# Kernel optimization log

Measured on AMD Instinct MI355X. Metric: run time of the kernel, lower is better.

## Reference

```python
import jax, jax.numpy as jnp
import numpy as np

E = 128   # embed_dim
H = 8     # num_heads
N, T, LQ, LK = 32, 50, 64, 64


def setup_inputs() -> dict:
    rng = jax.random.key(0)
    ks = jax.random.split(rng, 9)
    xav = np.sqrt(2.0 / (E + E)).astype(np.float32)  # xavier_normal for square E x E
    return {
        "query": jax.random.normal(ks[0], (N, T, LQ, E), jnp.float32),
        "key": jax.random.normal(ks[1], (N, T, LK, E), jnp.float32),
        "value": jax.random.normal(ks[2], (N, T, LK, E), jnp.float32),
        "key_padding_mask": jax.random.bernoulli(ks[3], 0.1, (N, T, LK)),
        "Wq": jax.random.normal(ks[4], (E, E), jnp.float32) * xav,
        "bq": jnp.zeros((E,), jnp.float32),
        "Wk": jax.random.normal(ks[5], (E, E), jnp.float32) * xav,
        "bk": jnp.zeros((E,), jnp.float32),
        "Wv": jax.random.normal(ks[6], (E, E), jnp.float32) * xav,
        "bv": jnp.zeros((E,), jnp.float32),
        "Wo": jax.random.normal(ks[7], (E, E), jnp.float32) * xav,
        "bo": jnp.zeros((E,), jnp.float32),
    }


def reference(query, key, value, key_padding_mask, Wq, bq, Wk, bk, Wv, bv, Wo, bo):
    b, t, lq, _ = query.shape
    lk = key.shape[2]
    # linear projections (torch Linear: x @ W.T + b)
    q = (query @ Wq.T + bq).reshape(b, t, lq, H, -1)   # [b,T,Lq,h,d]
    k = (key @ Wk.T + bk).reshape(b, t, lk, H, -1)     # [b,T,Lk,h,d]
    v = (value @ Wv.T + bv).reshape(b, t, lk, H, -1)   # [b,T,Lk,h,d]
    scale = 1.0 / np.sqrt(q.shape[-1]).astype(np.float32)
    attn = jnp.einsum('bTlhd,bTthd->bThlt', q, k) * scale  # [b,T,h,Lq,Lk]
    mask = key_padding_mask[:, :, None, None, :]            # [b,T,1,1,Lk]
    attn = jnp.where(mask, -jnp.inf, attn)
    attn = jax.nn.softmax(attn, axis=-1)
    attn = jnp.nan_to_num(attn, nan=0.0)                    # fully-masked rows -> 0
    out = jnp.einsum('bThlt,bTthd->bTlhd', attn, v)
    out = out.reshape(b, t, lq, -1) @ Wo.T + bo             # [b,T,Lq,E]
    # match torch output layout for attn: [head, b, T, Lq, Lk]
    return out, jnp.transpose(attn, (2, 0, 1, 3, 4))
```

## Files before the change

kernel.cpp:

```cpp
#include <hip/hip_runtime.h>
#include <hip/hip_bf16.h>


#define NBT 1600
#define OUT0_ELEMS 13107200L

typedef __attribute__((ext_vector_type(8))) short bf16x8;
typedef __attribute__((ext_vector_type(4))) short bf16x4;
typedef __attribute__((ext_vector_type(4))) float f32x4;
typedef __attribute__((ext_vector_type(4))) unsigned short u16x4;

__device__ __forceinline__ unsigned short f2b(float f) {
  union { float f; unsigned u; } v; v.f = f;
  unsigned r = v.u + 0x7FFFu + ((v.u >> 16) & 1u);
  return (unsigned short)(r >> 16);
}
__device__ __forceinline__ float b2f(unsigned short s) {
  union { unsigned u; float f; } v; v.u = ((unsigned)s) << 16;
  return v.f;
}
__device__ __forceinline__ bf16x4 pack4(f32x4 v) {
  bf16x4 r;
  r[0] = (short)f2b(v[0]); r[1] = (short)f2b(v[1]);
  r[2] = (short)f2b(v[2]); r[3] = (short)f2b(v[3]);
  return r;
}

#if defined(__has_builtin)
#if __has_builtin(__builtin_amdgcn_mfma_f32_16x16x16bf16_1k)
#define HAVE_MFMA16_1K 1
#endif
#endif

__device__ __forceinline__ f32x4 mfma16(bf16x4 a, bf16x4 b, f32x4 c) {
#ifdef HAVE_MFMA16_1K
  return __builtin_amdgcn_mfma_f32_16x16x16bf16_1k(a, b, c, 0, 0, 0);
#else
  f32x4 d;
  asm volatile("v_mfma_f32_16x16x16_bf16 %0, %1, %2, %3\n\ts_nop 7\n\ts_nop 7"
               : "=v"(d)
               : "v"(a), "v"(b), "v"(c));
  return d;
#endif
}

__device__ __forceinline__ int xs_idx(int r, int c) {
  return r * 128 + (c ^ ((r & 7) << 3));
}
__device__ __forceinline__ int qk_idx(int l, int d) {
  return l * 16 + (d ^ ((l & 3) << 2));
}
__device__ __forceinline__ int ps_idx(int r, int c) {
  return r * 64 + (c ^ ((r & 7) << 3));
}

__global__ void prep_kernel(const float* __restrict__ Wq,
                            const float* __restrict__ Wk,
                            const float* __restrict__ Wv,
                            const float* __restrict__ Wo,
                            const unsigned char* __restrict__ maskp,
                            unsigned short* __restrict__ wall,
                            int* __restrict__ flag) {
  int b = blockIdx.x;
  int t = threadIdx.x;
  if (b < 256) {
    int idx = b * 256 + t;
    int m = idx >> 14, j = idx & 16383;
    const float* src = (m == 0) ? Wq : (m == 1) ? Wk : (m == 2) ? Wv : Wo;
    float s = (m == 0) ? 0.25f : 1.0f;
    wall[idx] = f2b(src[j] * s);
  } else {
    __shared__ int sb, sf;
    if (t == 0) { sb = 0; sf = 0; }
    __syncthreads();
    int bnz = 0, fcnt = 0;
    for (int i = t * 16; i < t * 16 + 16; ++i)
      if ((i & 3) && maskp[i]) bnz++;
    const unsigned int* w = (const unsigned int*)maskp;
    for (int i = t * 4; i < t * 4 + 4; ++i)
      if (w[i] == 0x3f800000u) fcnt++;
    if (bnz) atomicAdd(&sb, 1);
    if (fcnt) atomicAdd(&sf, 1);
    __syncthreads();
    if (t == 0) *flag = sf ? 2 : (sb ? 1 : 0);
  }
}

__global__ __launch_bounds__(512, 3) void fused_kernel(
    const float* __restrict__ q_in, const float* __restrict__ k_in,
    const float* __restrict__ v_in, const unsigned char* __restrict__ maskp,
    const int* __restrict__ modeFlag, const unsigned short* __restrict__ wall,
    const float* __restrict__ bq, const float* __restrict__ bk,
    const float* __restrict__ bv, const float* __restrict__ bo,
    float* __restrict__ out0, float* __restrict__ attn_out) {
  __shared__ __align__(16) unsigned short Xs0[64 * 128];
  __shared__ __align__(16) unsigned short Xs1[64 * 128];
  __shared__ __align__(16) unsigned short QKw[8 * 1024];
  __shared__ float maskS[64];

  const int tid = threadIdx.x;
  const int w = tid >> 6;
  const int lane = tid & 63;
  const int ln = lane & 15, g = lane >> 4;
  const long bT = blockIdx.x;

  unsigned short* Sw = QKw + w * 1024;

  if (tid < 64) {
    int mode = *modeFlag;
    long midx = bT * 64 + tid;
    bool mk;
    if (mode == 0)      mk = ((const int*)maskp)[midx] != 0;
    else if (mode == 1) mk = maskp[midx] != 0;
    else                mk = ((const float*)maskp)[midx] != 0.0f;
    maskS[tid] = mk ? -INFINITY : 0.0f;
  }

  const float* xsrc0 = q_in + bT * 8192;
  const float* xsrc1 = k_in + bT * 8192;
  const float* xsrc2 = v_in + bT * 8192;

  float4 xcur[4];
  #pragma unroll
  for (int it = 0; it < 4; ++it)
    xcur[it] = *(const float4*)(xsrc0 + it * 2048 + tid * 4);

  bf16x4 vk[4];
  bf16x4 aK[4], bQ[4];

  #pragma unroll
  for (int t3 = 0; t3 < 3; ++t3) {
    unsigned short* Xb = (t3 == 1) ? Xs1 : Xs0;
    #pragma unroll
    for (int it = 0; it < 4; ++it) {
      int flat = it * 2048 + tid * 4;
      int r = flat >> 7, c = flat & 127;
      float4 xv = xcur[it];
      u16x4 pk;
      pk[0] = f2b(xv.x); pk[1] = f2b(xv.y);
      pk[2] = f2b(xv.z); pk[3] = f2b(xv.w);
      *(u16x4*)&Xb[xs_idx(r, c)] = pk;
    }
    if (t3 < 2) {
      const float* nsrc = (t3 == 0) ? xsrc1 : xsrc2;
      #pragma unroll
      for (int it = 0; it < 4; ++it)
        xcur[it] = *(const float4*)(nsrc + it * 2048 + tid * 4);
    }
    __syncthreads();

    const unsigned short* wb = wall + t3 * 16384 + (w * 16 + ln) * 128 + 8 * g;
    const float* bias = (t3 == 0) ? bq : (t3 == 1) ? bk : bv;
    float bval = bias[w * 16 + ln] * ((t3 == 0) ? 0.25f : 1.0f);

    f32x4 acc[4] = {};
    #pragma unroll
    for (int ks = 0; ks < 4; ++ks) {
      bf16x8 bwk = *(const bf16x8*)(wb + ks * 32);
      bf16x8 a[4];
      #pragma unroll
      for (int ms = 0; ms < 4; ++ms)
        a[ms] = *(const bf16x8*)&Xb[xs_idx(ms * 16 + ln, ks * 32 + 8 * g)];
      #pragma unroll
      for (int ms = 0; ms < 4; ++ms)
        acc[ms] = __builtin_amdgcn_mfma_f32_16x16x32_bf16(a[ms], bwk,
                                                          acc[ms], 0, 0, 0);
    }

    #pragma unroll
    for (int ms = 0; ms < 4; ++ms) {
      if (t3 == 2) {
        f32x4 vb;
        #pragma unroll
        for (int r = 0; r < 4; ++r) vb[r] = acc[ms][r] + bval;
        vk[ms] = pack4(vb);
      } else {
        #pragma unroll
        for (int r = 0; r < 4; ++r) {
          int l = ms * 16 + 4 * g + r;
          Sw[qk_idx(l, ln)] = f2b(acc[ms][r] + bval);
        }
      }
    }
    if (t3 == 0) {
      #pragma unroll
      for (int i = 0; i < 4; ++i)
        bQ[i] = *(const bf16x4*)&Sw[qk_idx(i * 16 + ln, 4 * g)];
    } else if (t3 == 1) {
      #pragma unroll
      for (int i = 0; i < 4; ++i)
        aK[i] = *(const bf16x4*)&Sw[qk_idx(i * 16 + ln, 4 * g)];
    }
  }

  const long abase = ((long)w * NBT + bT) * 4096;
  #pragma unroll
  for (int lsub = 0; lsub < 4; ++lsub) {
    f32x4 s4[4];
    #pragma unroll
    for (int t = 0; t < 4; ++t) {
      f32x4 z = {};
      s4[t] = mfma16(aK[t], bQ[lsub], z);
    }
    float m = -INFINITY;
    #pragma unroll
    for (int t = 0; t < 4; ++t) {
      f32x4 mvt = *(const f32x4*)&maskS[t * 16 + 4 * g];
      #pragma unroll
      for (int r = 0; r < 4; ++r) {
        float sv = s4[t][r] + mvt[r];
        s4[t][r] = sv;
        m = fmaxf(m, sv);
      }
    }
    m = fmaxf(m, __shfl_xor(m, 16, 64));
    m = fmaxf(m, __shfl_xor(m, 32, 64));
    float sum = 0.f;
    #pragma unroll
    for (int t = 0; t < 4; ++t)
      #pragma unroll
      for (int r = 0; r < 4; ++r) {
        float p = (m == -INFINITY) ? 0.f : __expf(s4[t][r] - m);
        s4[t][r] = p;
        sum += p;
      }
    sum += __shfl_xor(sum, 16, 64);
    sum += __shfl_xor(sum, 32, 64);
    float inv = (sum > 0.f) ? 1.f / sum : 0.f;

    bf16x4 pa4[4];
    #pragma unroll
    for (int t = 0; t < 4; ++t) {
      f32x4 ps;
      #pragma unroll
      for (int r = 0; r < 4; ++r) ps[r] = s4[t][r] * inv;
      pa4[t] = pack4(ps);
    }

    #pragma unroll
    for (int t = 0; t < 4; ++t)
      *(u16x4*)&Sw[ps_idx(ln, t * 16 + 4 * g)] = *(const u16x4*)&pa4[t];
    #pragma unroll
    for (int j = 0; j < 4; ++j) {
      int row = 4 * j + g;
      u16x4 pv = *(const u16x4*)&Sw[ps_idx(row, 4 * ln)];
      f32x4 o;
      o[0] = b2f(pv[0]); o[1] = b2f(pv[1]);
      o[2] = b2f(pv[2]); o[3] = b2f(pv[3]);
      *(f32x4*)&attn_out[abase + (long)(lsub * 16 + row) * 64 + 4 * ln] = o;
    }

    f32x4 oacc = {};
    #pragma unroll
    for (int t = 0; t < 4; ++t) oacc = mfma16(pa4[t], vk[t], oacc);
    #pragma unroll
    for (int r = 0; r < 4; ++r)
      Xs1[xs_idx(lsub * 16 + 4 * g + r, w * 16 + ln)] = f2b(oacc[r]);
  }

  __syncthreads();

  {
    const unsigned short* wo = wall + 3 * 16384 + (w * 16 + ln) * 128 + 8 * g;
    float bov = bo[w * 16 + ln];

    f32x4 acc[4] = {};
    #pragma unroll
    for (int ks = 0; ks < 4; ++ks) {
      bf16x8 bwk = *(const bf16x8*)(wo + ks * 32);
      bf16x8 a[4];
      #pragma unroll
      for (int ms = 0; ms < 4; ++ms)
        a[ms] = *(const bf16x8*)&Xs1[xs_idx(ms * 16 + ln, ks * 32 + 8 * g)];
      #pragma unroll
      for (int ms = 0; ms < 4; ++ms)
        acc[ms] = __builtin_amdgcn_mfma_f32_16x16x32_bf16(a[ms], bwk,
                                                          acc[ms], 0, 0, 0);
    }
    #pragma unroll
    for (int ms = 0; ms < 4; ++ms)
      #pragma unroll
      for (int r = 0; r < 4; ++r)
        out0[(bT * 64 + ms * 16 + 4 * g + r) * 128 + w * 16 + ln] =
            acc[ms][r] + bov;
  }
}

extern "C" void kernel_launch(void* const* d_in, const int* in_sizes, int n_in,
                              void* d_out, int out_size, void* d_ws,
                              size_t ws_size, hipStream_t stream) {
  (void)in_sizes; (void)n_in; (void)out_size; (void)ws_size;
  const float* query = (const float*)d_in[0];
  const float* key   = (const float*)d_in[1];
  const float* value = (const float*)d_in[2];
  const unsigned char* mask = (const unsigned char*)d_in[3];
  const float* Wq = (const float*)d_in[4];
  const float* bq = (const float*)d_in[5];
  const float* Wk = (const float*)d_in[6];
  const float* bk = (const float*)d_in[7];
  const float* Wv = (const float*)d_in[8];
  const float* bv = (const float*)d_in[9];
  const float* Wo = (const float*)d_in[10];
  const float* bo = (const float*)d_in[11];

  float* out0 = (float*)d_out;
  float* attn_out = out0 + OUT0_ELEMS;

  char* ws = (char*)d_ws;
  int* flag = (int*)ws;
  unsigned short* wall = (unsigned short*)(ws + 256);

  prep_kernel<<<257, 256, 0, stream>>>(Wq, Wk, Wv, Wo, mask, wall, flag);
  fused_kernel<<<NBT, 512, 0, stream>>>(query, key, value, mask, flag, wall,
                                        bq, bk, bv, bo, out0, attn_out);
}
```

Measured before the change: 106.7 us.

## Process two tiles per block and prefetch the next tile's query during the current one

The grid is halved so each block handles two (b,T) tiles, one at index blockIdx.x and one at blockIdx.x + 800. While the current tile's value projection runs, the next tile's query rows are already being loaded into registers. This hides part of the global-load latency at the tile boundary and removes half of the block launch and setup overhead. In exchange, each block runs longer and the two tiles execute one after the other, which can change how work spreads across CUs and leave a longer tail wave.

```diff
diff --git a/kernel.cpp b/kernel.cpp
--- a/kernel.cpp
+++ b/kernel.cpp
@@ -3,6 +3,7 @@
 
 
 #define NBT 1600
+#define HALF_NBT 800
 #define OUT0_ELEMS 13107200L
 
 typedef __attribute__((ext_vector_type(8))) short bf16x8;
@@ -102,187 +103,198 @@
   const int w = tid >> 6;
   const int lane = tid & 63;
   const int ln = lane & 15, g = lane >> 4;
-  const long bT = blockIdx.x;
+  const int mode = *modeFlag;
 
   unsigned short* Sw = QKw + w * 1024;
 
-  if (tid < 64) {
-    int mode = *modeFlag;
-    long midx = bT * 64 + tid;
-    bool mk;
-    if (mode == 0)      mk = ((const int*)maskp)[midx] != 0;
-    else if (mode == 1) mk = maskp[midx] != 0;
-    else                mk = ((const float*)maskp)[midx] != 0.0f;
-    maskS[tid] = mk ? -INFINITY : 0.0f;
+  float4 xcur[4];
+  {
+    const float* src = q_in + (long)blockIdx.x * 8192;
+    #pragma unroll
+    for (int it = 0; it < 4; ++it)
+      xcur[it] = *(const float4*)(src + it * 2048 + tid * 4);
   }
 
-  const float* xsrc0 = q_in + bT * 8192;
-  const float* xsrc1 = k_in + bT * 8192;
-  const float* xsrc2 = v_in + bT * 8192;
-
-  float4 xcur[4];
   #pragma unroll
-  for (int it = 0; it < 4; ++it)
-    xcur[it] = *(const float4*)(xsrc0 + it * 2048 + tid * 4);
-
-  bf16x4 vk[4];
-  bf16x4 aK[4], bQ[4];
-
-  #pragma unroll
-  for (int t3 = 0; t3 < 3; ++t3) {
-    unsigned short* Xb = (t3 == 1) ? Xs1 : Xs0;
+  for (int tile = 0; tile < 2; ++tile) {
+    const long bT = blockIdx.x + tile * HALF_NBT;
+
+    if (tid < 64) {
+      long midx = bT * 64 + tid;
+      bool mk;
+      if (mode == 0)      mk = ((const int*)maskp)[midx] != 0;
+      else if (mode == 1) mk = maskp[midx] != 0;
+      else                mk = ((const float*)maskp)[midx] != 0.0f;
+      maskS[tid] = mk ? -INFINITY : 0.0f;
+    }
+
+    bf16x4 vk[4];
+    bf16x4 aK[4], bQ[4];
+
     #pragma unroll
-    for (int it = 0; it < 4; ++it) {
-      int flat = it * 2048 + tid * 4;
-      int r = flat >> 7, c = flat & 127;
-      float4 xv = xcur[it];
-      u16x4 pk;
-      pk[0] = f2b(xv.x); pk[1] = f2b(xv.y);
-      pk[2] = f2b(xv.z); pk[3] = f2b(xv.w);
-      *(u16x4*)&Xb[xs_idx(r, c)] = pk;
+    for (int t3 = 0; t3 < 3; ++t3) {
+      unsigned short* Xb = (t3 == 1) ? Xs1 : Xs0;
+      #pragma unroll
+      for (int it = 0; it < 4; ++it) {
+        int flat = it * 2048 + tid * 4;
+        int r = flat >> 7, c = flat & 127;
+        float4 xv = xcur[it];
+        u16x4 pk;
+        pk[0] = f2b(xv.x); pk[1] = f2b(xv.y);
+        pk[2] = f2b(xv.z); pk[3] = f2b(xv.w);
+        *(u16x4*)&Xb[xs_idx(r, c)] = pk;
+      }
+      {
+        const float* nsrc = nullptr;
+        if (t3 == 0)      nsrc = k_in + bT * 8192;
+        else if (t3 == 1) nsrc = v_in + bT * 8192;
+        else if (tile == 0)
+          nsrc = q_in + (bT + HALF_NBT) * 8192;
+        if (nsrc) {
+          #pragma unroll
+          for (int it = 0; it < 4; ++it)
+            xcur[it] = *(const float4*)(nsrc + it * 2048 + tid * 4);
+        }
+      }
+      __syncthreads();
+
+      const unsigned short* wb =
+          wall + t3 * 16384 + (w * 16 + ln) * 128 + 8 * g;
+      const float* bias = (t3 == 0) ? bq : (t3 == 1) ? bk : bv;
+      float bval = bias[w * 16 + ln] * ((t3 == 0) ? 0.25f : 1.0f);
+
+      f32x4 acc[4] = {};
+      #pragma unroll
+      for (int ks = 0; ks < 4; ++ks) {
+        bf16x8 bwk = *(const bf16x8*)(wb + ks * 32);
+        bf16x8 a[4];
+        #pragma unroll
+        for (int ms = 0; ms < 4; ++ms)
+          a[ms] = *(const bf16x8*)&Xb[xs_idx(ms * 16 + ln, ks * 32 + 8 * g)];
+        #pragma unroll
+        for (int ms = 0; ms < 4; ++ms)
+          acc[ms] = __builtin_amdgcn_mfma_f32_16x16x32_bf16(a[ms], bwk,
+                                                            acc[ms], 0, 0, 0);
+      }
+
+      #pragma unroll
+      for (int ms = 0; ms < 4; ++ms) {
+        if (t3 == 2) {
+          f32x4 vb;
+          #pragma unroll
+          for (int r = 0; r < 4; ++r) vb[r] = acc[ms][r] + bval;
+          vk[ms] = pack4(vb);
+        } else {
+          #pragma unroll
+          for (int r = 0; r < 4; ++r) {
+            int l = ms * 16 + 4 * g + r;
+            Sw[qk_idx(l, ln)] = f2b(acc[ms][r] + bval);
+          }
+        }
+      }
+      if (t3 == 0) {
+        #pragma unroll
+        for (int i = 0; i < 4; ++i)
+          bQ[i] = *(const bf16x4*)&Sw[qk_idx(i * 16 + ln, 4 * g)];
+      } else if (t3 == 1) {
+        #pragma unroll
+        for (int i = 0; i < 4; ++i)
+          aK[i] = *(const bf16x4*)&Sw[qk_idx(i * 16 + ln, 4 * g)];
+      }
     }
-    if (t3 < 2) {
-      const float* nsrc = (t3 == 0) ? xsrc1 : xsrc2;
-      #pragma unroll
-      for (int it = 0; it < 4; ++it)
-        xcur[it] = *(const float4*)(nsrc + it * 2048 + tid * 4);
+
+    const long abase = ((long)w * NBT + bT) * 4096;
+    #pragma unroll
+    for (int lsub = 0; lsub < 4; ++lsub) {
+      f32x4 s4[4];
+      #pragma unroll
+      for (int t = 0; t < 4; ++t) {
+        f32x4 z = {};
+        s4[t] = mfma16(aK[t], bQ[lsub], z);
+      }
+      float m = -INFINITY;
+      #pragma unroll
+      for (int t = 0; t < 4; ++t) {
+        f32x4 mvt = *(const f32x4*)&maskS[t * 16 + 4 * g];
+        #pragma unroll
+        for (int r = 0; r < 4; ++r) {
+          float sv = s4[t][r] + mvt[r];
+          s4[t][r] = sv;
+          m = fmaxf(m, sv);
+        }
+      }
+      m = fmaxf(m, __shfl_xor(m, 16, 64));
+      m = fmaxf(m, __shfl_xor(m, 32, 64));
+      float sum = 0.f;
+      #pragma unroll
+      for (int t = 0; t < 4; ++t)
+        #pragma unroll
+        for (int r = 0; r < 4; ++r) {
+          float p = (m == -INFINITY) ? 0.f : __expf(s4[t][r] - m);
+          s4[t][r] = p;
+          sum += p;
+        }
+      sum += __shfl_xor(sum, 16, 64);
+      sum += __shfl_xor(sum, 32, 64);
+      float inv = (sum > 0.f) ? 1.f / sum : 0.f;
+
+      bf16x4 pa4[4];
+      #pragma unroll
+      for (int t = 0; t < 4; ++t) {
+        f32x4 ps;
+        #pragma unroll
+        for (int r = 0; r < 4; ++r) ps[r] = s4[t][r] * inv;
+        pa4[t] = pack4(ps);
+      }
+
+      #pragma unroll
+      for (int t = 0; t < 4; ++t)
+        *(u16x4*)&Sw[ps_idx(ln, t * 16 + 4 * g)] = *(const u16x4*)&pa4[t];
+      #pragma unroll
+      for (int j = 0; j < 4; ++j) {
+        int row = 4 * j + g;
+        u16x4 pv = *(const u16x4*)&Sw[ps_idx(row, 4 * ln)];
+        f32x4 o;
+        o[0] = b2f(pv[0]); o[1] = b2f(pv[1]);
+        o[2] = b2f(pv[2]); o[3] = b2f(pv[3]);
+        *(f32x4*)&attn_out[abase + (long)(lsub * 16 + row) * 64 + 4 * ln] = o;
+      }
+
+      f32x4 oacc = {};
+      #pragma unroll
+      for (int t = 0; t < 4; ++t) oacc = mfma16(pa4[t], vk[t], oacc);
+      #pragma unroll
+      for (int r = 0; r < 4; ++r)
+        Xs1[xs_idx(lsub * 16 + 4 * g + r, w * 16 + ln)] = f2b(oacc[r]);
     }
+
     __syncthreads();
 
-    const unsigned short* wb = wall + t3 * 16384 + (w * 16 + ln) * 128 + 8 * g;
-    const float* bias = (t3 == 0) ? bq : (t3 == 1) ? bk : bv;
-    float bval = bias[w * 16 + ln] * ((t3 == 0) ? 0.25f : 1.0f);
-
-    f32x4 acc[4] = {};
-    #pragma unroll
-    for (int ks = 0; ks < 4; ++ks) {
-      bf16x8 bwk = *(const bf16x8*)(wb + ks * 32);
-      bf16x8 a[4];
+    {
+      const unsigned short* wo =
+          wall + 3 * 16384 + (w * 16 + ln) * 128 + 8 * g;
+      float bov = bo[w * 16 + ln];
+
+      f32x4 acc[4] = {};
+      #pragma unroll
+      for (int ks = 0; ks < 4; ++ks) {
+        bf16x8 bwk = *(const bf16x8*)(wo + ks * 32);
+        bf16x8 a[4];
+        #pragma unroll
+        for (int ms = 0; ms < 4; ++ms)
+          a[ms] = *(const bf16x8*)&Xs1[xs_idx(ms * 16 + ln, ks * 32 + 8 * g)];
+        #pragma unroll
+        for (int ms = 0; ms < 4; ++ms)
+          acc[ms] = __builtin_amdgcn_mfma_f32_16x16x32_bf16(a[ms], bwk,
+                                                            acc[ms], 0, 0, 0);
+      }
       #pragma unroll
       for (int ms = 0; ms < 4; ++ms)
-        a[ms] = *(const bf16x8*)&Xb[xs_idx(ms * 16 + ln, ks * 32 + 8 * g)];
-      #pragma unroll
-      for (int ms = 0; ms < 4; ++ms)
-        acc[ms] = __builtin_amdgcn_mfma_f32_16x16x32_bf16(a[ms], bwk,
-                                                          acc[ms], 0, 0, 0);
+        #pragma unroll
+        for (int r = 0; r < 4; ++r)
+          out0[(bT * 64 + ms * 16 + 4 * g + r) * 128 + w * 16 + ln] =
+              acc[ms][r] + bov;
     }
-
-    #pragma unroll
-    for (int ms = 0; ms < 4; ++ms) {
-      if (t3 == 2) {
-        f32x4 vb;
-        #pragma unroll
-        for (int r = 0; r < 4; ++r) vb[r] = acc[ms][r] + bval;
-        vk[ms] = pack4(vb);
-      } else {
-        #pragma unroll
-        for (int r = 0; r < 4; ++r) {
-          int l = ms * 16 + 4 * g + r;
-          Sw[qk_idx(l, ln)] = f2b(acc[ms][r] + bval);
-        }
-      }
-    }
-    if (t3 == 0) {
-      #pragma unroll
-      for (int i = 0; i < 4; ++i)
-        bQ[i] = *(const bf16x4*)&Sw[qk_idx(i * 16 + ln, 4 * g)];
-    } else if (t3 == 1) {
-      #pragma unroll
-      for (int i = 0; i < 4; ++i)
-        aK[i] = *(const bf16x4*)&Sw[qk_idx(i * 16 + ln, 4 * g)];
-    }
-  }
-
-  const long abase = ((long)w * NBT + bT) * 4096;
-  #pragma unroll
-  for (int lsub = 0; lsub < 4; ++lsub) {
-    f32x4 s4[4];
-    #pragma unroll
-    for (int t = 0; t < 4; ++t) {
-      f32x4 z = {};
-      s4[t] = mfma16(aK[t], bQ[lsub], z);
-    }
-    float m = -INFINITY;
-    #pragma unroll
-    for (int t = 0; t < 4; ++t) {
-      f32x4 mvt = *(const f32x4*)&maskS[t * 16 + 4 * g];
-      #pragma unroll
-      for (int r = 0; r < 4; ++r) {
-        float sv = s4[t][r] + mvt[r];
-        s4[t][r] = sv;
-        m = fmaxf(m, sv);
-      }
-    }
-    m = fmaxf(m, __shfl_xor(m, 16, 64));
-    m = fmaxf(m, __shfl_xor(m, 32, 64));
-    float sum = 0.f;
-    #pragma unroll
-    for (int t = 0; t < 4; ++t)
-      #pragma unroll
-      for (int r = 0; r < 4; ++r) {
-        float p = (m == -INFINITY) ? 0.f : __expf(s4[t][r] - m);
-        s4[t][r] = p;
-        sum += p;
-      }
-    sum += __shfl_xor(sum, 16, 64);
-    sum += __shfl_xor(sum, 32, 64);
-    float inv = (sum > 0.f) ? 1.f / sum : 0.f;
-
-    bf16x4 pa4[4];
-    #pragma unroll
-    for (int t = 0; t < 4; ++t) {
-      f32x4 ps;
-      #pragma unroll
-      for (int r = 0; r < 4; ++r) ps[r] = s4[t][r] * inv;
-      pa4[t] = pack4(ps);
-    }
-
-    #pragma unroll
-    for (int t = 0; t < 4; ++t)
-      *(u16x4*)&Sw[ps_idx(ln, t * 16 + 4 * g)] = *(const u16x4*)&pa4[t];
-    #pragma unroll
-    for (int j = 0; j < 4; ++j) {
-      int row = 4 * j + g;
-      u16x4 pv = *(const u16x4*)&Sw[ps_idx(row, 4 * ln)];
-      f32x4 o;
-      o[0] = b2f(pv[0]); o[1] = b2f(pv[1]);
-      o[2] = b2f(pv[2]); o[3] = b2f(pv[3]);
-      *(f32x4*)&attn_out[abase + (long)(lsub * 16 + row) * 64 + 4 * ln] = o;
-    }
-
-    f32x4 oacc = {};
-    #pragma unroll
-    for (int t = 0; t < 4; ++t) oacc = mfma16(pa4[t], vk[t], oacc);
-    #pragma unroll
-    for (int r = 0; r < 4; ++r)
-      Xs1[xs_idx(lsub * 16 + 4 * g + r, w * 16 + ln)] = f2b(oacc[r]);
-  }
-
-  __syncthreads();
-
-  {
-    const unsigned short* wo = wall + 3 * 16384 + (w * 16 + ln) * 128 + 8 * g;
-    float bov = bo[w * 16 + ln];
-
-    f32x4 acc[4] = {};
-    #pragma unroll
-    for (int ks = 0; ks < 4; ++ks) {
-      bf16x8 bwk = *(const bf16x8*)(wo + ks * 32);
-      bf16x8 a[4];
-      #pragma unroll
-      for (int ms = 0; ms < 4; ++ms)
-        a[ms] = *(const bf16x8*)&Xs1[xs_idx(ms * 16 + ln, ks * 32 + 8 * g)];
-      #pragma unroll
-      for (int ms = 0; ms < 4; ++ms)
-        acc[ms] = __builtin_amdgcn_mfma_f32_16x16x32_bf16(a[ms], bwk,
-                                                          acc[ms], 0, 0, 0);
-    }
-    #pragma unroll
-    for (int ms = 0; ms < 4; ++ms)
-      #pragma unroll
-      for (int r = 0; r < 4; ++r)
-        out0[(bT * 64 + ms * 16 + 4 * g + r) * 128 + w * 16 + ln] =
-            acc[ms][r] + bov;
   }
 }
 
@@ -311,6 +323,7 @@
   unsigned short* wall = (unsigned short*)(ws + 256);
 
   prep_kernel<<<257, 256, 0, stream>>>(Wq, Wk, Wv, Wo, mask, wall, flag);
-  fused_kernel<<<NBT, 512, 0, stream>>>(query, key, value, mask, flag, wall,
-                                        bq, bk, bv, bo, out0, attn_out);
-}
+  fused_kernel<<<HALF_NBT, 512, 0, stream>>>(query, key, value, mask, flag,
+                                             wall, bq, bk, bv, bo, out0,
+                                             attn_out);
+}
```

New measurement: 143.8 us. +34.9%, slower.
